# Kernel tuning notes

Hardware: AMD Instinct MI355X
Metric: run time of the kernel (lower is better)

## Reference

```python
import jax, jax.numpy as jnp
import numpy as np

B, N, E, Q = 4, 10000, 160000, 256
D, M, U, H, P = 128, 64, 126, 128, 7  # node_dim, msg_sz, update_sz, mlp hidden, pose dim
MSG_STEPS = 3
NUM_COPIES = 1


def setup_inputs() -> dict:
    key = jax.random.key(0)
    ks = jax.random.split(key, 12)
    return {
        "nodes_states": jax.random.normal(ks[0], (B, N, D), jnp.float32),
        "query_poses": jax.random.normal(ks[1], (B, Q, P), jnp.float32),
        "attn": jax.random.uniform(ks[2], (B, Q, N), jnp.float32) / N,
        "edge_sources": jax.random.randint(ks[3], (E,), 0, N),
        "edge_sinks": jax.random.randint(ks[4], (E,), 0, N),
        "w1e": jax.random.normal(ks[5], (2 * D, H), jnp.float32) * 0.05,
        "b1e": jnp.zeros((H,), jnp.float32),
        "w2e": jax.random.normal(ks[6], (H, M), jnp.float32) * 0.05,
        "b2e": jnp.zeros((M,), jnp.float32),
        "w1n": jax.random.normal(ks[7], (D + M, H), jnp.float32) * 0.05,
        "b1n": jnp.zeros((H,), jnp.float32),
        "w2n": jax.random.normal(ks[8], (H, U), jnp.float32) * 0.05,
        "b2n": jnp.zeros((U,), jnp.float32),
    }


def reference(nodes_states, query_poses, attn, edge_sources, edge_sinks,
              w1e, b1e, w2e, b2e, w1n, b1n, w2n, b2n):
    def step(states, _):
        # gather endpoint states: [B, E, 2*D]
        einp = jnp.concatenate([states[:, edge_sources], states[:, edge_sinks]], axis=-1)
        # edge MLP -> per-edge messages [B, E, M]
        msg = jax.nn.relu(einp @ w1e + b1e) @ w2e + b2e
        # scatter-add messages to sink nodes [B, N, M]
        incoming = jnp.zeros((states.shape[0], N, M), states.dtype).at[:, edge_sinks].add(msg)
        # node MLP update [B, N, U]
        ninp = jnp.concatenate([incoming, states], axis=-1)
        upd = jax.nn.relu(ninp @ w1n + b1n) @ w2n + b2n
        # only the last U channels (state part, not positions) are updated
        states = states.at[:, :, -U:].add(upd)
        return states, None

    states, _ = jax.lax.scan(step, nodes_states, None, length=MSG_STEPS)
    extraction = jnp.einsum('bqn,bnd->bqd', attn, states)  # interpolation readout
    return jnp.concatenate([query_poses] * NUM_COPIES + [extraction], axis=-1)
```

## Files before the change

kernel.cpp:

```cpp
#include <hip/hip_runtime.h>

#define Bx 4
#define Nn 10000
#define Ee 160000
#define Qq 256
#define Dd 128
#define Mm 64
#define Uu 126
#define Hh 128
#define Pp 7

#define KG 1252

typedef unsigned short u16;
typedef __bf16 bf16x8 __attribute__((ext_vector_type(8)));
typedef float f32x4 __attribute__((ext_vector_type(4)));

__device__ __forceinline__ float b2f(u16 h){
  unsigned u = ((unsigned)h) << 16; float f; __builtin_memcpy(&f, &u, 4); return f;
}
__device__ __forceinline__ u16 f2b(float f){
  __bf16 h = (__bf16)f; u16 r; __builtin_memcpy(&r, &h, 2); return r;
}
__device__ __forceinline__ float ldin(const void* p, long i, int flag){
  return flag ? b2f(((const u16*)p)[i]) : ((const float*)p)[i];
}

__global__ void probe_kernel(const void* in0, int* flag){
  if (threadIdx.x == 0 && blockIdx.x == 0){
    const u16* p = (const u16*)in0;
    int cnt = 0;
    for (int i = 0; i < 256; i++){
      float a = fabsf(b2f(p[i]));
      if (a > 0.0009765625f && a < 32.0f) cnt++;
    }
    *flag = (cnt >= 240) ? 1 : 0;
  }
}

__global__ void prep_kernel(const void* w1e, const void* b1e, const void* w2e, const void* b2e,
                            const void* w1n, const void* b1n, const void* w2n, const void* b2n,
                            const int* __restrict__ flag,
                            u16* w1e_s, u16* w2e_s, u16* w1n_s, u16* w2n_s,
                            float* b1e_f, float* b2e_f, float* b1n_f, float* b2n_f)
{
  int f = *flag;
  for (int idx = blockIdx.x * blockDim.x + threadIdx.x; idx < 82368; idx += gridDim.x * blockDim.x){
    if (idx < 32768){
      int k = idx >> 7, h = idx & 127;
      w1e_s[(k >> 3) * 1024 + h * 8 + (k & 7)] = f2b(ldin(w1e, idx, f));
    } else if (idx < 40960){
      int i2 = idx - 32768; int k = i2 >> 6, m2 = i2 & 63;
      w2e_s[(k >> 3) * 512 + m2 * 8 + (k & 7)] = f2b(ldin(w2e, i2, f));
    } else if (idx < 65536){
      int i2 = idx - 40960; int k = i2 >> 7, h = i2 & 127;
      w1n_s[(k >> 3) * 1024 + h * 8 + (k & 7)] = f2b(ldin(w1n, i2, f));
    } else if (idx < 81920){
      int i2 = idx - 65536; int k = i2 >> 7, u = i2 & 127;
      float v = (u < 126) ? ldin(w2n, (long)k * 126 + u, f) : 0.f;
      w2n_s[(k >> 3) * 1024 + u * 8 + (k & 7)] = f2b(v);
    } else if (idx < 82048){ b1e_f[idx - 81920] = ldin(b1e, idx - 81920, f); }
    else if (idx < 82112){ b2e_f[idx - 82048] = ldin(b2e, idx - 82048, f); }
    else if (idx < 82240){ b1n_f[idx - 82112] = ldin(b1n, idx - 82112, f); }
    else { int j = idx - 82240; b2n_f[j] = (j < 126) ? ldin(b2n, j, f) : 0.f; }
  }
}

__global__ void init_states_kernel(const void* in0, const int* __restrict__ flag,
                                   const int* __restrict__ snk,
                                   float* __restrict__ sf, u16* __restrict__ sbm,
                                   int* __restrict__ cnt)
{
  int f = *flag;
  const long total = (long)Bx * Nn * Dd;
  long base = (long)blockIdx.x * blockDim.x + threadIdx.x;
  for (long i = base; i < total; i += (long)gridDim.x * blockDim.x){
    float v = ldin(in0, i, f);
    sf[i] = v; sbm[i] = f2b(v);
  }
  for (long i = base; i < Ee; i += (long)gridDim.x * blockDim.x)
    atomicAdd(&cnt[snk[(int)i]], 1);
}

__global__ void scan_kernel(const int* __restrict__ cnt, int* __restrict__ rowp){
  __shared__ int tot[1024];
  int t = threadIdx.x;
  int base = t * 10;
  int local[10]; int s = 0;
  #pragma unroll
  for (int i = 0; i < 10; i++){
    int v = (base + i < Nn) ? cnt[base + i] : 0;
    local[i] = s; s += v;
  }
  tot[t] = s;
  __syncthreads();
  for (int o = 1; o < 1024; o <<= 1){
    int v = (t >= o) ? tot[t - o] : 0;
    __syncthreads();
    tot[t] += v;
    __syncthreads();
  }
  int prefix = (t == 0) ? 0 : tot[t - 1];
  #pragma unroll
  for (int i = 0; i < 10; i++)
    if (base + i < Nn) rowp[base + i] = prefix + local[i];
  if (t == 1023) rowp[Nn] = tot[1023];
}
__global__ void fill_kernel(const int* __restrict__ src, const int* __restrict__ snk,
                            const int* __restrict__ rowp, int* __restrict__ cnt,
                            int* __restrict__ psrc){
  int i = blockIdx.x * blockDim.x + threadIdx.x;
  if (i < Ee){
    int s = snk[i];
    int p = rowp[s] + atomicAdd(&cnt[s], 1);
    psrc[p] = src[i];
  }
}

__global__ __launch_bounds__(256) void xform_kernel(
  const u16* __restrict__ sbm, const u16* __restrict__ w1s,
  const float* __restrict__ b1f, u16* __restrict__ xab)
{
  __shared__ __align__(16) u16 w1h[16384];
  __shared__ __align__(16) u16 Yt[64 * 136];
  int tid = threadIdx.x;
  int b = (blockIdx.x & 7) >> 1;
  int nt = ((blockIdx.x >> 3) << 1) + (blockIdx.x & 1);
  if (nt >= 157) return;
  int n0 = nt * 64;
  int w = tid >> 6, lane = tid & 63, m = lane & 15, quad = lane >> 4;
  int n = n0 + w * 16 + m;
  int nld = n < Nn ? n : Nn - 1;
  const u16* srow = sbm + (((size_t)b * Nn + nld) << 7);

  bf16x8 a[4];
  #pragma unroll
  for (int lk = 0; lk < 4; lk++) a[lk] = *(const bf16x8*)(srow + lk * 32 + quad * 8);

  const f32x4 z4 = {0.f, 0.f, 0.f, 0.f};
  int row_l = lane >> 2, seg = lane & 3;
  int nst = n0 + w * 16 + row_l;

  #pragma unroll
  for (int half = 0; half < 2; half++){
    __syncthreads();
    {
      const uint4* g = (const uint4*)(w1s + half * 16384);
      uint4* l = (uint4*)w1h;
      #pragma unroll
      for (int i = 0; i < 8; i++) l[tid + i * 256] = g[tid + i * 256];
    }
    __syncthreads();
    f32x4 acc[8];
    #pragma unroll
    for (int ct = 0; ct < 8; ct++) acc[ct] = z4;
    #pragma unroll
    for (int lk = 0; lk < 4; lk++){
      #pragma unroll
      for (int ct = 0; ct < 8; ct++){
        bf16x8 bv = *(const bf16x8*)(w1h + (((lk * 4 + quad) << 7) + ct * 16 + m) * 8);
        acc[ct] = __builtin_amdgcn_mfma_f32_16x16x32_bf16(a[lk], bv, acc[ct], 0, 0, 0);
      }
    }
    #pragma unroll
    for (int ct = 0; ct < 8; ct++){
      float bb = (half == 0) ? b1f[ct * 16 + m] : 0.f;
      #pragma unroll
      for (int i = 0; i < 4; i++)
        Yt[(w * 16 + quad * 4 + i) * 136 + ct * 16 + m] = f2b(acc[ct][i] + bb);
    }
    if (nst < Nn){
      const u16* tb = Yt + (w * 16 + row_l) * 136 + seg * 8;
      uint4 x0 = *(const uint4*)(tb);
      uint4 x1 = *(const uint4*)(tb + 32);
      uint4 x2 = *(const uint4*)(tb + 64);
      uint4 x3 = *(const uint4*)(tb + 96);
      u16* gb = xab + ((size_t)b * Nn + nst) * 256 + half * 128 + seg * 8;
      *(uint4*)(gb)      = x0;
      *(uint4*)(gb + 32) = x1;
      *(uint4*)(gb + 64) = x2;
      *(uint4*)(gb + 96) = x3;
    }
  }
}

__global__ __launch_bounds__(256) void node_kernel(
  float* __restrict__ sf, u16* __restrict__ sbm, const u16* __restrict__ xab,
  const int* __restrict__ rowp, const int* __restrict__ psrc,
  const u16* __restrict__ w2es, const float* __restrict__ b2ef,
  const u16* __restrict__ w1s, const u16* __restrict__ w2s,
  const float* __restrict__ b1f, const float* __restrict__ b2f2)
{
  __shared__ __align__(16) u16 ninp[64 * 200];
  __shared__ __align__(16) u16 hsYt[64 * 136];
  int b = (blockIdx.x & 7) >> 1;
  int nt = ((blockIdx.x >> 3) << 1) + (blockIdx.x & 1);
  if (nt >= 157) return;
  int n0 = nt * 64;
  int tid = threadIdx.x;

  {
    int nl = tid >> 2, part = tid & 3;
    int n = n0 + nl;
    float acc[32];
    #pragma unroll
    for (int i = 0; i < 32; i++) acc[i] = 0.f;
    if (n < Nn){
      float xbf[32];
      {
        const u16* xp = xab + ((size_t)b * Nn + n) * 256 + 128 + part * 8;
        union { uint4 v; u16 h[8]; } q[4];
        q[0].v = *(const uint4*)(xp);
        q[1].v = *(const uint4*)(xp + 32);
        q[2].v = *(const uint4*)(xp + 64);
        q[3].v = *(const uint4*)(xp + 96);
        #pragma unroll
        for (int t4 = 0; t4 < 4; t4++)
          #pragma unroll
          for (int j = 0; j < 8; j++) xbf[t4 * 8 + j] = b2f(q[t4].h[j]);
      }
      int r0 = rowp[n], r1 = rowp[n + 1];
      const u16* xb0 = xab + (size_t)b * Nn * 256 + part * 8;
      for (int r = r0; r < r1; r++){
        int s = psrc[r];
        const u16* xs = xb0 + (size_t)s * 256;
        union { uint4 v; u16 h[8]; } q[4];
        q[0].v = *(const uint4*)(xs);
        q[1].v = *(const uint4*)(xs + 32);
        q[2].v = *(const uint4*)(xs + 64);
        q[3].v = *(const uint4*)(xs + 96);
        #pragma unroll
        for (int t4 = 0; t4 < 4; t4++)
          #pragma unroll
          for (int j = 0; j < 8; j++){
            float v = b2f(q[t4].h[j]) + xbf[t4 * 8 + j];
            acc[t4 * 8 + j] += v > 0.f ? v : 0.f;
          }
      }
    }
    union { u16 h[32]; uint4 v[4]; } hb;
    #pragma unroll
    for (int i = 0; i < 32; i++) hb.h[i] = f2b(acc[i]);
    u16* hp = hsYt + nl * 136 + part * 8;
    *(uint4*)(hp)      = hb.v[0];
    *(uint4*)(hp + 32) = hb.v[1];
    *(uint4*)(hp + 64) = hb.v[2];
    *(uint4*)(hp + 96) = hb.v[3];
    u16* dp = ninp + nl * 200 + 64 + part * 8;
    if (n < Nn){
      const u16* sp = sbm + (((size_t)b * Nn + n) << 7) + part * 8;
      *(uint4*)(dp)      = *(const uint4*)(sp);
      *(uint4*)(dp + 32) = *(const uint4*)(sp + 32);
      *(uint4*)(dp + 64) = *(const uint4*)(sp + 64);
      *(uint4*)(dp + 96) = *(const uint4*)(sp + 96);
    } else {
      uint4 zz = {0, 0, 0, 0};
      *(uint4*)(dp)      = zz;
      *(uint4*)(dp + 32) = zz;
      *(uint4*)(dp + 64) = zz;
      *(uint4*)(dp + 96) = zz;
    }
  }

  int w = tid >> 6, lane = tid & 63, m = lane & 15, quad = lane >> 4;
  const f32x4 z4 = {0.f, 0.f, 0.f, 0.f};

  {
    f32x4 acc[4];
    #pragma unroll
    for (int ct = 0; ct < 4; ct++) acc[ct] = z4;
    #pragma unroll
    for (int ks = 0; ks < 4; ks++){
      bf16x8 a = *(const bf16x8*)(hsYt + (w * 16 + m) * 136 + ks * 32 + quad * 8);
      #pragma unroll
      for (int ct = 0; ct < 4; ct++){
        bf16x8 bv = *(const bf16x8*)(w2es + (((ks * 4 + quad) << 6) + ct * 16 + m) * 8);
        acc[ct] = __builtin_amdgcn_mfma_f32_16x16x32_bf16(a, bv, acc[ct], 0, 0, 0);
      }
    }
    #pragma unroll
    for (int i = 0; i < 4; i++){
      int n = n0 + w * 16 + quad * 4 + i;
      float deg = (n < Nn) ? (float)(rowp[n + 1] - rowp[n]) : 0.f;
      #pragma unroll
      for (int ct = 0; ct < 4; ct++)
        ninp[(w * 16 + quad * 4 + i) * 200 + ct * 16 + m] = f2b(acc[ct][i] + deg * b2ef[ct * 16 + m]);
    }
  }

  f32x4 acc1[8];
  #pragma unroll
  for (int ct = 0; ct < 8; ct++) acc1[ct] = z4;
  #pragma unroll 1
  for (int ks = 0; ks < 6; ks++){
    bf16x8 a = *(const bf16x8*)(ninp + (w * 16 + m) * 200 + ks * 32 + quad * 8);
    #pragma unroll
    for (int ct = 0; ct < 8; ct++){
      bf16x8 bv = *(const bf16x8*)(w1s + (((ks * 4 + quad) << 7) + ct * 16 + m) * 8);
      acc1[ct] = __builtin_amdgcn_mfma_f32_16x16x32_bf16(a, bv, acc1[ct], 0, 0, 0);
    }
  }
  #pragma unroll
  for (int ct = 0; ct < 8; ct++){
    float bb = b1f[ct * 16 + m];
    #pragma unroll
    for (int i = 0; i < 4; i++){
      float v = acc1[ct][i] + bb;
      v = v > 0.f ? v : 0.f;
      hsYt[(w * 16 + quad * 4 + i) * 136 + ct * 16 + m] = f2b(v);
    }
  }
  f32x4 acc2[8];
  #pragma unroll
  for (int ct = 0; ct < 8; ct++) acc2[ct] = z4;
  #pragma unroll 1
  for (int ko = 0; ko < 4; ko++){
    bf16x8 a2 = *(const bf16x8*)(hsYt + (w * 16 + m) * 136 + ko * 32 + quad * 8);
    #pragma unroll
    for (int ct = 0; ct < 8; ct++){
      bf16x8 bv = *(const bf16x8*)(w2s + (((ko * 4 + quad) << 7) + ct * 16 + m) * 8);
      acc2[ct] = __builtin_amdgcn_mfma_f32_16x16x32_bf16(a2, bv, acc2[ct], 0, 0, 0);
    }
  }
  #pragma unroll
  for (int ct = 0; ct < 8; ct++){
    int u = ct * 16 + m;
    if (u < 126){
      float bb = b2f2[u];
      #pragma unroll
      for (int i = 0; i < 4; i++){
        int n = n0 + w * 16 + quad * 4 + i;
        if (n < Nn){
          size_t idx = (((size_t)b * Nn + n) << 7) + 2 + u;
          float v = sf[idx] + acc2[ct][i] + bb;
          sf[idx] = v;
          sbm[idx] = f2b(v);
        }
      }
    }
  }
}

__global__ void swz_s_kernel(const u16* __restrict__ sbm, u16* __restrict__ sswz)
{
  const long total = (long)Bx * KG * 128;
  for (long i = (long)blockIdx.x * blockDim.x + threadIdx.x; i < total; i += (long)gridDim.x * blockDim.x){
    int d = (int)(i & 127); long r = i >> 7;
    int kg = (int)(r % KG); int b = (int)(r / KG);
    union { u16 h[8]; uint4 v[2]; } t;
    if (kg < 1250){
      #pragma unroll
      for (int j = 0; j < 8; j++)
        t.h[j] = sbm[(((size_t)b * Nn + kg * 8 + j) << 7) + d];
    } else {
      #pragma unroll
      for (int j = 0; j < 8; j++) t.h[j] = 0;
    }
    *(uint4*)(sswz + i * 8) = t.v[0];
    *(uint4*)(sswz + i * 8 + 8) = t.v[1];
  }
}
__global__ __launch_bounds__(256) void extract2_kernel(
  const void* __restrict__ attn, const int* __restrict__ flag,
  const u16* __restrict__ sswz, float* __restrict__ part)
{
  int f = *flag;
  int blk = blockIdx.x;
  int kc = blk & 31, qt = (blk >> 5) & 3, b = blk >> 7;
  int tid = threadIdx.x, w = tid >> 6, lane = tid & 63, m = lane & 15, quad = lane >> 4;
  int qr = qt * 4 + w, q0 = qr * 16;
  int kg0 = kc * 40;
  int nsteps = (kc == 31) ? 3 : 10;
  long arow = ((long)(b * Qq + q0 + m)) * Nn;
  const u16* ab16 = (const u16*)attn + arow;
  const float* af32 = (const float*)attn + arow;
  const u16* sbase = sswz + ((size_t)b) * KG * 1024;
  f32x4 acc[8];
  const f32x4 z4 = {0.f, 0.f, 0.f, 0.f};
  #pragma unroll
  for (int ct = 0; ct < 8; ct++) acc[ct] = z4;
  #pragma unroll 1
  for (int t = 0; t < nsteps; t++){
    int kg = kg0 + t * 4 + quad;
    int kgc = kg < KG ? kg : 0;
    bf16x8 a;
    if (kg < 1250){
      if (f){
        a = *(const bf16x8*)(ab16 + kg * 8);
      } else {
        const float* ap = af32 + kg * 8;
        float4 p0 = *(const float4*)ap;
        float4 p1 = *(const float4*)(ap + 4);
        a[0] = (__bf16)p0.x; a[1] = (__bf16)p0.y; a[2] = (__bf16)p0.z; a[3] = (__bf16)p0.w;
        a[4] = (__bf16)p1.x; a[5] = (__bf16)p1.y; a[6] = (__bf16)p1.z; a[7] = (__bf16)p1.w;
      }
    } else {
      #pragma unroll
      for (int j = 0; j < 8; j++) a[j] = (__bf16)0.f;
    }
    #pragma unroll
    for (int ct = 0; ct < 8; ct++){
      bf16x8 bv = *(const bf16x8*)(sbase + ((size_t)kgc * 128 + ct * 16 + m) * 8);
      acc[ct] = __builtin_amdgcn_mfma_f32_16x16x32_bf16(a, bv, acc[ct], 0, 0, 0);
    }
  }
  #pragma unroll
  for (int ct = 0; ct < 8; ct++){
    #pragma unroll
    for (int i = 0; i < 4; i++)
      part[(((size_t)(kc * 4 + b)) * Qq + q0 + quad * 4 + i) * 128 + ct * 16 + m] = acc[ct][i];
  }
}

__global__ void final_kernel(const void* __restrict__ poses, const int* __restrict__ flag,
                             const float* __restrict__ part, void* __restrict__ out)
{
  int f = *flag;
  const long total = (long)Bx * Qq * (Pp + Dd);
  for (long idx = (long)blockIdx.x * blockDim.x + threadIdx.x; idx < total; idx += (long)gridDim.x * blockDim.x){
    int j = (int)(idx % (Pp + Dd));
    long bq = idx / (Pp + Dd);
    float v;
    if (j < Pp){
      v = ldin(poses, bq * Pp + j, f);
    } else {
      int dd = j - Pp;
      int b = (int)(bq >> 8), q = (int)(bq & 255);
      v = 0.f;
      #pragma unroll
      for (int kc = 0; kc < 32; kc++)
        v += part[(((size_t)(kc * 4 + b) * Qq + q) << 7) + dd];
    }
    if (f) ((u16*)out)[idx] = f2b(v);
    else ((float*)out)[idx] = v;
  }
}

extern "C" void kernel_launch(void* const* d_in, const int* in_sizes, int n_in,
                              void* d_out, int out_size, void* d_ws, size_t ws_size,
                              hipStream_t stream)
{
  const void* in_states = d_in[0];
  const void* in_poses  = d_in[1];
  const void* in_attn   = d_in[2];
  const int*  in_src    = (const int*)d_in[3];
  const int*  in_snk    = (const int*)d_in[4];
  const void* in_w1e = d_in[5];  const void* in_b1e = d_in[6];
  const void* in_w2e = d_in[7];  const void* in_b2e = d_in[8];
  const void* in_w1n = d_in[9];  const void* in_b1n = d_in[10];
  const void* in_w2n = d_in[11]; const void* in_b2n = d_in[12];

  char* ws = (char*)d_ws;
  size_t off = 0;
  auto alloc = [&](size_t bytes){ size_t o = off; off = (off + bytes + 255) & ~(size_t)255; return o; };
  size_t o_sf   = alloc((size_t)Bx * Nn * Dd * 4);
  size_t o_sb   = alloc((size_t)Bx * Nn * Dd * 2);
  size_t o_xab  = alloc((size_t)Bx * Nn * 256 * 2);
  size_t o_rowp = alloc((size_t)(Nn + 1) * 4);
  size_t o_rcnt = alloc((size_t)Nn * 4);
  size_t o_psrc = alloc((size_t)Ee * 4);
  size_t o_w1e  = alloc(32768 * 2);
  size_t o_w2e  = alloc(8192 * 2);
  size_t o_w1n  = alloc(24576 * 2);
  size_t o_w2n  = alloc(16384 * 2);
  size_t o_b1e  = alloc(128 * 4);
  size_t o_b2e  = alloc(64 * 4);
  size_t o_b1n  = alloc(128 * 4);
  size_t o_b2n  = alloc(128 * 4);
  size_t o_flag = alloc(4);

  size_t sswzB = (size_t)Bx * KG * 128 * 8 * 2;
  size_t partB = (size_t)32 * Bx * Qq * Dd * 4;
  size_t o_sswz = alloc(sswzB);
  size_t o_part = alloc(partB);

  float* sf    = (float*)(ws + o_sf);
  u16*   sbm   = (u16*)(ws + o_sb);
  u16*   xab   = (u16*)(ws + o_xab);
  int*   rowp  = (int*)(ws + o_rowp);
  int*   rcnt  = (int*)(ws + o_rcnt);
  int*   psrc  = (int*)(ws + o_psrc);
  u16*   w1e_s = (u16*)(ws + o_w1e);
  u16*   w2e_s = (u16*)(ws + o_w2e);
  u16*   w1n_s = (u16*)(ws + o_w1n);
  u16*   w2n_s = (u16*)(ws + o_w2n);
  float* b1e_f = (float*)(ws + o_b1e);
  float* b2e_f = (float*)(ws + o_b2e);
  float* b1n_f = (float*)(ws + o_b1n);
  float* b2n_f = (float*)(ws + o_b2n);
  int*   flag  = (int*)(ws + o_flag);
  u16*   sswz  = (u16*)(ws + o_sswz);
  float* part  = (float*)(ws + o_part);

  hipMemsetAsync(rcnt, 0, (size_t)Nn * 4, stream);
  probe_kernel<<<1, 64, 0, stream>>>(in_states, flag);
  prep_kernel<<<322, 256, 0, stream>>>(in_w1e, in_b1e, in_w2e, in_b2e,
                                       in_w1n, in_b1n, in_w2n, in_b2n, flag,
                                       w1e_s, w2e_s, w1n_s, w2n_s,
                                       b1e_f, b2e_f, b1n_f, b2n_f);
  init_states_kernel<<<1024, 256, 0, stream>>>(in_states, flag, in_snk, sf, sbm, rcnt);

  scan_kernel<<<1, 1024, 0, stream>>>(rcnt, rowp);
  hipMemsetAsync(rcnt, 0, (size_t)Nn * 4, stream);
  fill_kernel<<<(Ee + 255) / 256, 256, 0, stream>>>(in_src, in_snk, rowp, rcnt, psrc);

  for (int step = 0; step < 3; step++){
    xform_kernel<<<632, 256, 0, stream>>>(sbm, w1e_s, b1e_f, xab);
    node_kernel<<<632, 256, 0, stream>>>(sf, sbm, xab, rowp, psrc,
                                         w2e_s, b2e_f,
                                         w1n_s, w2n_s, b1n_f, b2n_f);
  }
  swz_s_kernel<<<2504, 256, 0, stream>>>(sbm, sswz);
  extract2_kernel<<<512, 256, 0, stream>>>(in_attn, flag, sswz, part);
  final_kernel<<<540, 256, 0, stream>>>(in_poses, flag, part, d_out);
}
```

Measured before the change: 363.1 us.

## Fuse prep/init kernels, drop memset, tile swizzle through LDS, reorder gather loop

Merges the weight-prep and state-init kernels into one launch. A second count buffer, cleared by the single up-front memset, replaces the mid-pipeline memset. The state-swizzle kernel now stages 64-node tiles in shared memory so global reads are coalesced before transposing. The edge-gather inner loop is restructured into four independent unions, which may help scheduling. Together these aim to cut launch overhead and the strided global reads of the swizzle step.

New measurement: 358.1 us. No clear change (-1.4%).

```diff
diff --git a/kernel.cpp b/kernel.cpp
--- a/kernel.cpp
+++ b/kernel.cpp
@@ -38,47 +38,43 @@
   }
 }
 
-__global__ void prep_kernel(const void* w1e, const void* b1e, const void* w2e, const void* b2e,
-                            const void* w1n, const void* b1n, const void* w2n, const void* b2n,
-                            const int* __restrict__ flag,
-                            u16* w1e_s, u16* w2e_s, u16* w1n_s, u16* w2n_s,
-                            float* b1e_f, float* b2e_f, float* b1n_f, float* b2n_f)
+__global__ void prep_init_kernel(const void* w1e, const void* b1e, const void* w2e, const void* b2e,
+                                 const void* w1n, const void* b1n, const void* w2n, const void* b2n,
+                                 const void* in0, const int* __restrict__ snk,
+                                 const int* __restrict__ flag,
+                                 u16* w1e_s, u16* w2e_s, u16* w1n_s, u16* w2n_s,
+                                 float* b1e_f, float* b2e_f, float* b1n_f, float* b2n_f,
+                                 float* __restrict__ sf, u16* __restrict__ sbm,
+                                 int* __restrict__ cnt)
 {
   int f = *flag;
-  for (int idx = blockIdx.x * blockDim.x + threadIdx.x; idx < 82368; idx += gridDim.x * blockDim.x){
+  long gsz = (long)gridDim.x * blockDim.x;
+  long base = (long)blockIdx.x * blockDim.x + threadIdx.x;
+  for (long idx = base; idx < 82368; idx += gsz){
     if (idx < 32768){
-      int k = idx >> 7, h = idx & 127;
+      int k = (int)idx >> 7, h = (int)idx & 127;
       w1e_s[(k >> 3) * 1024 + h * 8 + (k & 7)] = f2b(ldin(w1e, idx, f));
     } else if (idx < 40960){
-      int i2 = idx - 32768; int k = i2 >> 6, m2 = i2 & 63;
+      int i2 = (int)idx - 32768; int k = i2 >> 6, m2 = i2 & 63;
       w2e_s[(k >> 3) * 512 + m2 * 8 + (k & 7)] = f2b(ldin(w2e, i2, f));
     } else if (idx < 65536){
-      int i2 = idx - 40960; int k = i2 >> 7, h = i2 & 127;
+      int i2 = (int)idx - 40960; int k = i2 >> 7, h = i2 & 127;
       w1n_s[(k >> 3) * 1024 + h * 8 + (k & 7)] = f2b(ldin(w1n, i2, f));
     } else if (idx < 81920){
-      int i2 = idx - 65536; int k = i2 >> 7, u = i2 & 127;
+      int i2 = (int)idx - 65536; int k = i2 >> 7, u = i2 & 127;
       float v = (u < 126) ? ldin(w2n, (long)k * 126 + u, f) : 0.f;
       w2n_s[(k >> 3) * 1024 + u * 8 + (k & 7)] = f2b(v);
     } else if (idx < 82048){ b1e_f[idx - 81920] = ldin(b1e, idx - 81920, f); }
     else if (idx < 82112){ b2e_f[idx - 82048] = ldin(b2e, idx - 82048, f); }
     else if (idx < 82240){ b1n_f[idx - 82112] = ldin(b1n, idx - 82112, f); }
-    else { int j = idx - 82240; b2n_f[j] = (j < 126) ? ldin(b2n, j, f) : 0.f; }
-  }
-}
-
-__global__ void init_states_kernel(const void* in0, const int* __restrict__ flag,
-                                   const int* __restrict__ snk,
-                                   float* __restrict__ sf, u16* __restrict__ sbm,
-                                   int* __restrict__ cnt)
-{
-  int f = *flag;
+    else { int j = (int)idx - 82240; b2n_f[j] = (j < 126) ? ldin(b2n, j, f) : 0.f; }
+  }
   const long total = (long)Bx * Nn * Dd;
-  long base = (long)blockIdx.x * blockDim.x + threadIdx.x;
-  for (long i = base; i < total; i += (long)gridDim.x * blockDim.x){
+  for (long i = base; i < total; i += gsz){
     float v = ldin(in0, i, f);
     sf[i] = v; sbm[i] = f2b(v);
   }
-  for (long i = base; i < Ee; i += (long)gridDim.x * blockDim.x)
+  for (long i = base; i < Ee; i += gsz)
     atomicAdd(&cnt[snk[(int)i]], 1);
 }
 
@@ -209,33 +205,38 @@
       float xbf[32];
       {
         const u16* xp = xab + ((size_t)b * Nn + n) * 256 + 128 + part * 8;
-        union { uint4 v; u16 h[8]; } q[4];
-        q[0].v = *(const uint4*)(xp);
-        q[1].v = *(const uint4*)(xp + 32);
-        q[2].v = *(const uint4*)(xp + 64);
-        q[3].v = *(const uint4*)(xp + 96);
+        union { uint4 v; u16 h[8]; } q0, q1, q2, q3;
+        q0.v = *(const uint4*)(xp);
+        q1.v = *(const uint4*)(xp + 32);
+        q2.v = *(const uint4*)(xp + 64);
+        q3.v = *(const uint4*)(xp + 96);
         #pragma unroll
-        for (int t4 = 0; t4 < 4; t4++)
-          #pragma unroll
-          for (int j = 0; j < 8; j++) xbf[t4 * 8 + j] = b2f(q[t4].h[j]);
+        for (int j = 0; j < 8; j++){
+          xbf[j] = b2f(q0.h[j]); xbf[8 + j] = b2f(q1.h[j]);
+          xbf[16 + j] = b2f(q2.h[j]); xbf[24 + j] = b2f(q3.h[j]);
+        }
       }
       int r0 = rowp[n], r1 = rowp[n + 1];
       const u16* xb0 = xab + (size_t)b * Nn * 256 + part * 8;
       for (int r = r0; r < r1; r++){
         int s = psrc[r];
         const u16* xs = xb0 + (size_t)s * 256;
-        union { uint4 v; u16 h[8]; } q[4];
-        q[0].v = *(const uint4*)(xs);
-        q[1].v = *(const uint4*)(xs + 32);
-        q[2].v = *(const uint4*)(xs + 64);
-        q[3].v = *(const uint4*)(xs + 96);
+        union { uint4 v; u16 h[8]; } q0, q1, q2, q3;
+        q0.v = *(const uint4*)(xs);
+        q1.v = *(const uint4*)(xs + 32);
+        q2.v = *(const uint4*)(xs + 64);
+        q3.v = *(const uint4*)(xs + 96);
         #pragma unroll
-        for (int t4 = 0; t4 < 4; t4++)
-          #pragma unroll
-          for (int j = 0; j < 8; j++){
-            float v = b2f(q[t4].h[j]) + xbf[t4 * 8 + j];
-            acc[t4 * 8 + j] += v > 0.f ? v : 0.f;
-          }
+        for (int j = 0; j < 8; j++){
+          float v0 = b2f(q0.h[j]) + xbf[j];
+          acc[j] += v0 > 0.f ? v0 : 0.f;
+          float v1 = b2f(q1.h[j]) + xbf[8 + j];
+          acc[8 + j] += v1 > 0.f ? v1 : 0.f;
+          float v2 = b2f(q2.h[j]) + xbf[16 + j];
+          acc[16 + j] += v2 > 0.f ? v2 : 0.f;
+          float v3 = b2f(q3.h[j]) + xbf[24 + j];
+          acc[24 + j] += v3 > 0.f ? v3 : 0.f;
+        }
       }
     }
     union { u16 h[32]; uint4 v[4]; } hb;
@@ -341,23 +342,38 @@
   }
 }
 
-__global__ void swz_s_kernel(const u16* __restrict__ sbm, u16* __restrict__ sswz)
-{
-  const long total = (long)Bx * KG * 128;
-  for (long i = (long)blockIdx.x * blockDim.x + threadIdx.x; i < total; i += (long)gridDim.x * blockDim.x){
-    int d = (int)(i & 127); long r = i >> 7;
-    int kg = (int)(r % KG); int b = (int)(r / KG);
-    union { u16 h[8]; uint4 v[2]; } t;
-    if (kg < 1250){
-      #pragma unroll
-      for (int j = 0; j < 8; j++)
-        t.h[j] = sbm[(((size_t)b * Nn + kg * 8 + j) << 7) + d];
-    } else {
-      #pragma unroll
-      for (int j = 0; j < 8; j++) t.h[j] = 0;
-    }
-    *(uint4*)(sswz + i * 8) = t.v[0];
-    *(uint4*)(sswz + i * 8 + 8) = t.v[1];
+__global__ __launch_bounds__(256) void swz_s_kernel(const u16* __restrict__ sbm, u16* __restrict__ sswz)
+{
+  __shared__ __align__(16) u16 tile[64 * 128];
+  int blk = blockIdx.x;
+  int b = blk & 3, nt = blk >> 2;
+  int n0 = nt * 64;
+  int t = threadIdx.x;
+  {
+    int row = t >> 2, s4 = (t & 3) * 4;
+    int n = n0 + row;
+    const uint4 z = {0, 0, 0, 0};
+    const u16* gp = sbm + (((size_t)b * Nn + (n < Nn ? n : 0)) << 7);
+    #pragma unroll
+    for (int s = 0; s < 4; s++){
+      uint4 v = (n < Nn) ? *(const uint4*)(gp + (s4 + s) * 8) : z;
+      *(uint4*)(tile + row * 128 + (s4 + s) * 8) = v;
+    }
+  }
+  __syncthreads();
+  int kgl = t >> 5;
+  int kg = nt * 8 + kgl;
+  if (kg < KG){
+    #pragma unroll
+    for (int o = 0; o < 4; o++){
+      int d = (t & 31) + o * 32;
+      union { u16 h[8]; uint4 v[2]; } r;
+      #pragma unroll
+      for (int j = 0; j < 8; j++) r.h[j] = tile[(kgl * 8 + j) * 128 + d];
+      u16* op = sswz + (((size_t)b * KG + kg) * 128 + d) * 8;
+      *(uint4*)(op)     = r.v[0];
+      *(uint4*)(op + 8) = r.v[1];
+    }
   }
 }
 __global__ __launch_bounds__(256) void extract2_kernel(
@@ -457,7 +473,7 @@
   size_t o_sb   = alloc((size_t)Bx * Nn * Dd * 2);
   size_t o_xab  = alloc((size_t)Bx * Nn * 256 * 2);
   size_t o_rowp = alloc((size_t)(Nn + 1) * 4);
-  size_t o_rcnt = alloc((size_t)Nn * 4);
+  size_t o_rcnt = alloc((size_t)Nn * 2 * 4);
   size_t o_psrc = alloc((size_t)Ee * 4);
   size_t o_w1e  = alloc(32768 * 2);
   size_t o_w2e  = alloc(8192 * 2);
@@ -479,6 +495,7 @@
   u16*   xab   = (u16*)(ws + o_xab);
   int*   rowp  = (int*)(ws + o_rowp);
   int*   rcnt  = (int*)(ws + o_rcnt);
+  int*   rcnt2 = rcnt + Nn;
   int*   psrc  = (int*)(ws + o_psrc);
   u16*   w1e_s = (u16*)(ws + o_w1e);
   u16*   w2e_s = (u16*)(ws + o_w2e);
@@ -492,17 +509,16 @@
   u16*   sswz  = (u16*)(ws + o_sswz);
   float* part  = (float*)(ws + o_part);
 
-  hipMemsetAsync(rcnt, 0, (size_t)Nn * 4, stream);
+  hipMemsetAsync(rcnt, 0, (size_t)Nn * 2 * 4, stream);
   probe_kernel<<<1, 64, 0, stream>>>(in_states, flag);
-  prep_kernel<<<322, 256, 0, stream>>>(in_w1e, in_b1e, in_w2e, in_b2e,
-                                       in_w1n, in_b1n, in_w2n, in_b2n, flag,
-                                       w1e_s, w2e_s, w1n_s, w2n_s,
-                                       b1e_f, b2e_f, b1n_f, b2n_f);
-  init_states_kernel<<<1024, 256, 0, stream>>>(in_states, flag, in_snk, sf, sbm, rcnt);
-
+  prep_init_kernel<<<1024, 256, 0, stream>>>(in_w1e, in_b1e, in_w2e, in_b2e,
+                                             in_w1n, in_b1n, in_w2n, in_b2n,
+                                             in_states, in_snk, flag,
+                                             w1e_s, w2e_s, w1n_s, w2n_s,
+                                             b1e_f, b2e_f, b1n_f, b2n_f,
+                                             sf, sbm, rcnt);
   scan_kernel<<<1, 1024, 0, stream>>>(rcnt, rowp);
-  hipMemsetAsync(rcnt, 0, (size_t)Nn * 4, stream);
-  fill_kernel<<<(Ee + 255) / 256, 256, 0, stream>>>(in_src, in_snk, rowp, rcnt, psrc);
+  fill_kernel<<<(Ee + 255) / 256, 256, 0, stream>>>(in_src, in_snk, rowp, rcnt2, psrc);
 
   for (int step = 0; step < 3; step++){
     xform_kernel<<<632, 256, 0, stream>>>(sbm, w1e_s, b1e_f, xab);
@@ -510,7 +526,7 @@
                                          w2e_s, b2e_f,
                                          w1n_s, w2n_s, b1n_f, b2n_f);
   }
-  swz_s_kernel<<<2504, 256, 0, stream>>>(sbm, sswz);
+  swz_s_kernel<<<628, 256, 0, stream>>>(sbm, sswz);
   extract2_kernel<<<512, 256, 0, stream>>>(in_attn, flag, sswz, part);
   final_kernel<<<540, 256, 0, stream>>>(in_poses, flag, part, d_out);
 }
```
